# Performance work log

Hardware: AMD Instinct MI355X
Metric: run time of the kernel (lower is better)

## Reference

```python
import jax, jax.numpy as jnp
import numpy as np

GAMMA = 0.8
THRES_CON = 0.95
EPS = 1e-6


def setup_inputs() -> dict:
    key = jax.random.key(0)
    k1, k2, k3, k4 = jax.random.split(key, 4)
    B, K, H, W, N = 16, 17, 256, 256, 4
    masks = jax.random.normal(k1, (B, 1, H, W), jnp.float32)
    pred_flows = jax.random.normal(k2, (N, B, 2, H, W), jnp.float32)
    skls = jax.random.randint(k3, (B, K, 2), 0, W).astype(jnp.int32)
    flows = jax.random.normal(k4, (B, 2, H, W), jnp.float32)
    return {"masks": masks, "pred_flows": pred_flows, "skls": skls, "flows": flows}


def _bce_with_logits(x, z):
    # mean of max(x,0) - x*z + log(1+exp(-|x|))  (numerically stable BCEWithLogits)
    return jnp.mean(jnp.maximum(x, 0.0) - x * z + jax.nn.softplus(-jnp.abs(x)))


def _con_loss(masks, pred_flow, which_kp, kp_flow, thres):
    # pred_flow: [B,2,H,W], kp_flow: [B,K,2], which_kp: [B,H,W]
    dots = jnp.einsum('bchw,bkc->bkhw', pred_flow, kp_flow)
    pn = jnp.linalg.norm(pred_flow, axis=1)            # [B,H,W]
    kn = jnp.linalg.norm(kp_flow, axis=-1)             # [B,K]
    sims = dots / (pn[:, None] * kn[:, :, None, None] + EPS)   # [B,K,H,W]
    sim_sel = jnp.take_along_axis(sims, which_kp[:, None], axis=1)  # [B,1,H,W]
    mask_gt = (sim_sel > thres).astype(jnp.float32)
    return _bce_with_logits(masks, mask_gt), mask_gt


def reference(masks, pred_flows, skls, flows):
    N = pred_flows.shape[0]
    B, _, H, W = flows.shape
    # nearest-keypoint assignment (depends only on skls, shared across iterations)
    iy, ix = jnp.meshgrid(jnp.arange(H, dtype=jnp.float32),
                          jnp.arange(W, dtype=jnp.float32), indexing='ij')
    kp = skls.astype(jnp.float32)                      # [B,K,2] (x,y)
    dis = (ix[None, None] - kp[..., 0, None, None]) ** 2 + \
          (iy[None, None] - kp[..., 1, None, None]) ** 2   # [B,K,H,W]
    which_kp = jnp.argmin(dis, axis=1)                 # [B,H,W]
    # gather gt flow vector at each keypoint: flow[b, :, y, x] -> [B,K,2]
    bidx = jnp.arange(B)[:, None]
    kp_flow = flows[bidx, :, skls[..., 1], skls[..., 0]]
    weights = [GAMMA ** (N - i - 1) for i in range(N)]
    loss = jnp.float32(0.0)
    mask_gt = None
    for i in range(N):
        l, mask_gt = _con_loss(masks, pred_flows[i], which_kp, kp_flow, THRES_CON)
        loss = loss + weights[i] * l
    return loss, mask_gt
```

## Files before the change

### kernel.cpp

```cpp
#include <hip/hip_runtime.h>
#include <math.h>

#define B 16
#define K 17
#define H 256
#define W 256
#define N 4
#define HW (H * W)
#define PPT 2
#define NBLK (B * (HW / (256 * PPT)))

__global__ __launch_bounds__(256) void conseg_kernel(
    const float* __restrict__ masks,
    const float* __restrict__ pred_flows,
    const int* __restrict__ skls,
    const float* __restrict__ flows,
    float* __restrict__ out,
    float* __restrict__ partials)
{
#pragma clang fp contract(off)
    __shared__ int   sx[K], sy[K];
    __shared__ float kfx[K], kfy[K], knrm[K];

    const int b   = blockIdx.x >> 7;
    const int tid = threadIdx.x;

    if (tid < K) {
        const int x = skls[(b * K + tid) * 2 + 0];
        const int y = skls[(b * K + tid) * 2 + 1];
        sx[tid] = x;
        sy[tid] = y;
        const float fx = flows[((b * 2 + 0) * H + y) * W + x];
        const float fy = flows[((b * 2 + 1) * H + y) * W + x];
        kfx[tid]  = fx;
        kfy[tid]  = fy;
        knrm[tid] = sqrtf(fx * fx + fy * fy);
    }
    __syncthreads();

    const int pix0 = ((blockIdx.x & 127) << 9) + tid * PPT;
    const int h    = pix0 >> 8;
    const int w0   = pix0 & 255;

    const float2 xm = *(const float2*)(masks + (size_t)b * HW + pix0);

    const size_t base = (size_t)b * 2 * HW + pix0;
    float2 px[N], py[N];
#pragma unroll
    for (int i = 0; i < N; ++i) {
        px[i] = *(const float2*)(pred_flows + (size_t)i * B * 2 * HW + base);
        py[i] = *(const float2*)(pred_flows + (size_t)i * B * 2 * HW + base + HW);
    }

    int best[PPT];
    int bestd[PPT];
#pragma unroll
    for (int j = 0; j < PPT; ++j) { best[j] = 0; bestd[j] = 0x7fffffff; }
#pragma unroll
    for (int k = 0; k < K; ++k) {
        const int kx = sx[k];
        const int dy = h - sy[k];
        const int dyy = dy * dy;
#pragma unroll
        for (int j = 0; j < PPT; ++j) {
            const int dx = (w0 + j) - kx;
            const int d  = dx * dx + dyy;
            if (d < bestd[j]) { bestd[j] = d; best[j] = k; }
        }
    }

    const float wts[N] = {0.512f, 0.64f, 0.8f, 1.0f};
    const float wsumc  = 0.512f + 0.64f + 0.8f + 1.0f;

    float acc = 0.0f;
    float zout[PPT];
#pragma unroll
    for (int j = 0; j < PPT; ++j) {
        const float kx  = kfx[best[j]];
        const float ky  = kfy[best[j]];
        const float knv = knrm[best[j]];

        const float x  = ((const float*)&xm)[j];
        const float sp = fmaxf(x, 0.0f) + log1pf(expf(-fabsf(x)));
        acc += wsumc * sp;

        float zlast = 0.0f;
#pragma unroll
        for (int i = 0; i < N; ++i) {
            const float pxv = ((const float*)&px[i])[j];
            const float pyv = ((const float*)&py[i])[j];
            const float dot = pxv * kx + pyv * ky;
            const float pn  = sqrtf(pxv * pxv + pyv * pyv);
            const float sim = dot / (pn * knv + 1e-6f);
            const float z   = (sim > 0.95f) ? 1.0f : 0.0f;
            acc -= wts[i] * (x * z);
            zlast = z;
        }
        zout[j] = zlast;
    }

    float* og = out + 1 + (size_t)b * HW + pix0;
#pragma unroll
    for (int j = 0; j < PPT; ++j) __builtin_nontemporal_store(zout[j], og + j);

    for (int off = 32; off > 0; off >>= 1)
        acc += __shfl_down(acc, off, 64);

    __shared__ float wsum[4];
    if ((tid & 63) == 0) wsum[tid >> 6] = acc;
    __syncthreads();
    if (tid == 0)
        partials[blockIdx.x] = wsum[0] + wsum[1] + wsum[2] + wsum[3];
}

__global__ __launch_bounds__(256) void conseg_reduce(
    const float* __restrict__ partials, float* __restrict__ out)
{
    const int tid = threadIdx.x;
    float s = 0.0f;
#pragma unroll
    for (int i = 0; i < NBLK / 256; ++i)
        s += partials[tid + i * 256];
    for (int off = 32; off > 0; off >>= 1)
        s += __shfl_down(s, off, 64);

    __shared__ float wsum[4];
    if ((tid & 63) == 0) wsum[tid >> 6] = s;
    __syncthreads();
    if (tid == 0)
        out[0] = (wsum[0] + wsum[1] + wsum[2] + wsum[3]) * (1.0f / (float)(B * HW));
}

extern "C" void kernel_launch(void* const* d_in, const int* in_sizes, int n_in,
                              void* d_out, int out_size, void* d_ws, size_t ws_size,
                              hipStream_t stream) {
    const float* masks      = (const float*)d_in[0];
    const float* pred_flows = (const float*)d_in[1];
    const int*   skls       = (const int*)d_in[2];
    const float* flows      = (const float*)d_in[3];
    float* out      = (float*)d_out;
    float* partials = (float*)d_ws;

    conseg_kernel<<<NBLK, 256, 0, stream>>>(masks, pred_flows, skls, flows, out, partials);
    conseg_reduce<<<1, 256, 0, stream>>>(partials, out);
}
```

Measured before the change: 18.25 us.

## Replace shared-memory keypoint table with per-lane registers and wave shuffles

Drops the shared-memory keypoint setup and its __syncthreads. Each lane now loads one keypoint's flow vector and norm, every thread reads all keypoints through scalar-uniform loads, and the chosen keypoint's values are fetched with __shfl. The argmin is packed into one integer min (distance shifted left by 5, OR'd with the index), and log1pf/expf are swapped for the fast __logf/__expf intrinsics. This removes the block barrier and the LDS round trip, at the cost of more redundant global loads and slightly different softplus precision.

```diff
diff --git a/kernel.cpp b/kernel.cpp
--- a/kernel.cpp
+++ b/kernel.cpp
@@ -19,31 +19,21 @@
     float* __restrict__ partials)
 {
 #pragma clang fp contract(off)
-    __shared__ int   sx[K], sy[K];
-    __shared__ float kfx[K], kfy[K], knrm[K];
+    const int b    = blockIdx.x >> 7;
+    const int tid  = threadIdx.x;
+    const int lane = tid & 63;
 
-    const int b   = blockIdx.x >> 7;
-    const int tid = threadIdx.x;
-
-    if (tid < K) {
-        const int x = skls[(b * K + tid) * 2 + 0];
-        const int y = skls[(b * K + tid) * 2 + 1];
-        sx[tid] = x;
-        sy[tid] = y;
-        const float fx = flows[((b * 2 + 0) * H + y) * W + x];
-        const float fy = flows[((b * 2 + 1) * H + y) * W + x];
-        kfx[tid]  = fx;
-        kfy[tid]  = fy;
-        knrm[tid] = sqrtf(fx * fx + fy * fy);
-    }
-    __syncthreads();
+    const int  lk  = min(lane, K - 1);
+    const int2 kpl = ((const int2*)skls)[b * K + lk];
+    const float kfx = flows[((size_t)(b * 2 + 0) * H + kpl.y) * W + kpl.x];
+    const float kfy = flows[((size_t)(b * 2 + 1) * H + kpl.y) * W + kpl.x];
+    const float kkn = sqrtf(kfx * kfx + kfy * kfy);
 
     const int pix0 = ((blockIdx.x & 127) << 9) + tid * PPT;
     const int h    = pix0 >> 8;
     const int w0   = pix0 & 255;
 
     const float2 xm = *(const float2*)(masks + (size_t)b * HW + pix0);
-
     const size_t base = (size_t)b * 2 * HW + pix0;
     float2 px[N], py[N];
 #pragma unroll
@@ -52,56 +42,66 @@
         py[i] = *(const float2*)(pred_flows + (size_t)i * B * 2 * HW + base + HW);
     }
 
-    int best[PPT];
-    int bestd[PPT];
+    int2 kp[K];
 #pragma unroll
-    for (int j = 0; j < PPT; ++j) { best[j] = 0; bestd[j] = 0x7fffffff; }
+    for (int k = 0; k < K; ++k) kp[k] = ((const int2*)skls)[b * K + k];
+
+    int best0 = 0x7fffffff, best1 = 0x7fffffff;
 #pragma unroll
     for (int k = 0; k < K; ++k) {
-        const int kx = sx[k];
-        const int dy = h - sy[k];
+        const int dy  = h - kp[k].y;
         const int dyy = dy * dy;
+        const int dx0 = w0 - kp[k].x;
+        const int dx1 = dx0 + 1;
+        const int d0  = dx0 * dx0 + dyy;
+        const int d1  = dx1 * dx1 + dyy;
+        best0 = min(best0, (d0 << 5) | k);
+        best1 = min(best1, (d1 << 5) | k);
+    }
+    const int k0 = best0 & 31;
+    const int k1 = best1 & 31;
+
+    const float kx0 = __shfl(kfx, k0), ky0 = __shfl(kfy, k0), kn0 = __shfl(kkn, k0);
+    const float kx1 = __shfl(kfx, k1), ky1 = __shfl(kfy, k1), kn1 = __shfl(kkn, k1);
+
+    const float wts[N] = {0.512f, 0.64f, 0.8f, 1.0f};
+    float acc = 0.0f;
+    float z0 = 0.0f, z1 = 0.0f;
+
+    {
+        const float x  = xm.x;
+        const float sp = fmaxf(x, 0.0f) + __logf(1.0f + __expf(-fabsf(x)));
+        acc += 2.952f * sp;
 #pragma unroll
-        for (int j = 0; j < PPT; ++j) {
-            const int dx = (w0 + j) - kx;
-            const int d  = dx * dx + dyy;
-            if (d < bestd[j]) { bestd[j] = d; best[j] = k; }
+        for (int i = 0; i < N; ++i) {
+            const float pxv = px[i].x, pyv = py[i].x;
+            const float dot = pxv * kx0 + pyv * ky0;
+            const float pn  = sqrtf(pxv * pxv + pyv * pyv);
+            const float sim = dot / (pn * kn0 + 1e-6f);
+            const float z   = (sim > 0.95f) ? 1.0f : 0.0f;
+            acc -= wts[i] * (x * z);
+            z0 = z;
+        }
+    }
+    {
+        const float x  = xm.y;
+        const float sp = fmaxf(x, 0.0f) + __logf(1.0f + __expf(-fabsf(x)));
+        acc += 2.952f * sp;
+#pragma unroll
+        for (int i = 0; i < N; ++i) {
+            const float pxv = px[i].y, pyv = py[i].y;
+            const float dot = pxv * kx1 + pyv * ky1;
+            const float pn  = sqrtf(pxv * pxv + pyv * pyv);
+            const float sim = dot / (pn * kn1 + 1e-6f);
+            const float z   = (sim > 0.95f) ? 1.0f : 0.0f;
+            acc -= wts[i] * (x * z);
+            z1 = z;
         }
     }
 
-    const float wts[N] = {0.512f, 0.64f, 0.8f, 1.0f};
-    const float wsumc  = 0.512f + 0.64f + 0.8f + 1.0f;
-
-    float acc = 0.0f;
-    float zout[PPT];
-#pragma unroll
-    for (int j = 0; j < PPT; ++j) {
-        const float kx  = kfx[best[j]];
-        const float ky  = kfy[best[j]];
-        const float knv = knrm[best[j]];
-
-        const float x  = ((const float*)&xm)[j];
-        const float sp = fmaxf(x, 0.0f) + log1pf(expf(-fabsf(x)));
-        acc += wsumc * sp;
-
-        float zlast = 0.0f;
-#pragma unroll
-        for (int i = 0; i < N; ++i) {
-            const float pxv = ((const float*)&px[i])[j];
-            const float pyv = ((const float*)&py[i])[j];
-            const float dot = pxv * kx + pyv * ky;
-            const float pn  = sqrtf(pxv * pxv + pyv * pyv);
-            const float sim = dot / (pn * knv + 1e-6f);
-            const float z   = (sim > 0.95f) ? 1.0f : 0.0f;
-            acc -= wts[i] * (x * z);
-            zlast = z;
-        }
-        zout[j] = zlast;
-    }
-
     float* og = out + 1 + (size_t)b * HW + pix0;
-#pragma unroll
-    for (int j = 0; j < PPT; ++j) __builtin_nontemporal_store(zout[j], og + j);
+    __builtin_nontemporal_store(z0, og + 0);
+    __builtin_nontemporal_store(z1, og + 1);
 
     for (int off = 32; off > 0; off >>= 1)
         acc += __shfl_down(acc, off, 64);
```

Measured after the change: 16.81 us. 7.9% less time.
